# Kernel tuning notes

Measured on AMD Instinct MI355X. Metric: run time of the kernel, lower is better.

## Reference

```python
import jax, jax.numpy as jnp
import numpy as np

P, B, N, K = 8, 256, 512, 64
RHO = 0.999

def setup_inputs() -> dict:
    key = jax.random.key(0)
    k1, k2, k3, k4, k5, k6 = jax.random.split(key, 6)
    return {
        "WL": jax.random.normal(k1, (P, B, N, K), dtype=jnp.float32) * 0.05,
        "WR": jax.random.normal(k2, (P, B, K, N), dtype=jnp.float32) * 0.05,
        "v_tm1": jax.random.normal(k3, (B, N), dtype=jnp.float32),
        "v_t": jax.random.normal(k4, (B, N), dtype=jnp.float32),
        "ac_idx": jax.random.randint(k5, (B,), 0, P, dtype=jnp.int32),
        "pc_mask": jax.random.randint(k6, (B, P), 0, 2, dtype=jnp.int32),
    }

def reference(WL, WR, v_tm1, v_t, ac_idx, pc_mask):
    # constants from rehebbian(): n = x.shape[-1]*rho**2, g = 0.5*(log(1+r)-log(1-r))/r
    n = N * RHO ** 2
    g = 0.5 * (np.log(1.0 + RHO) - np.log(1.0 - RHO)) / RHO

    # ---- per-example pathway gather + batched low-rank matvec + tanh (tick v update) ----
    b_idx = jnp.arange(B)
    WL_sel = WL[ac_idx, b_idx]            # [B, N, K]
    WR_sel = WR[ac_idx, b_idx]            # [B, K, N]
    Wx = jnp.einsum("bkn,bn->bk", WR_sel, v_t)      # [B, K]
    v_next = jnp.tanh(jnp.einsum("bnk,bk->bn", WL_sel, Wx))  # [B, N]

    # ---- rehebbian rank-1 growth for every pathway, gated per example ----
    WRx = jnp.einsum("pbkn,bn->pbk", WR, v_tm1)      # [P, B, K]
    WLWRx = jnp.einsum("pbnk,pbk->pbn", WL, WRx)     # [P, B, N]
    mask = pc_mask.T.astype(WL.dtype)[:, :, None]    # [P, B, 1]
    dWL = ((g * v_t[None, :, :] - WLWRx) * mask)[..., None]          # [P, B, N, 1]
    dWR = (v_tm1[None, :, None, :] / n) * mask[..., None]            # [P, B, 1, N]
    return v_next, dWL, dWR
```

## Files before the change

kernel.cpp:

```cpp
#include <hip/hip_runtime.h>
#include <math.h>

#define GP 8
#define GB 256
#define GN 512
#define GK 64

__device__ __forceinline__ void fma4(float4& acc, const float4 a, const float4 b) {
    acc.x += a.x * b.x; acc.y += a.y * b.y; acc.z += a.z * b.z; acc.w += a.w * b.w;
}
__device__ __forceinline__ float hsum4(const float4 a) {
    return (a.x + a.y) + (a.z + a.w);
}

__global__ __launch_bounds__(256, 4) void ghu_fused(
    const float* __restrict__ WL,
    const float* __restrict__ WR,
    const float* __restrict__ v_tm1,
    const float* __restrict__ v_t,
    const int*   __restrict__ ac_idx,
    const int*   __restrict__ pc_mask,
    float* __restrict__ out,
    float g, float inv_n)
{
    const int b    = blockIdx.x;
    const int p    = blockIdx.y;
    const int tid  = threadIdx.x;
    const int wave = tid >> 6;
    const int lane = tid & 63;
    const int sub  = lane & 3;
    const int rsub = lane >> 2;

    __shared__ float s_vtm1[GN];
    __shared__ float s_vt[GN];
    __shared__ float s_WRx[GK];
    __shared__ float s_Wx[GK];
    __shared__ float s_dWL[GN];
    __shared__ float s_vnext[GN];

    s_vtm1[tid]       = v_tm1[b * GN + tid];
    s_vtm1[tid + 256] = v_tm1[b * GN + tid + 256];
    s_vt[tid]         = v_t[b * GN + tid];
    s_vt[tid + 256]   = v_t[b * GN + tid + 256];
    __syncthreads();

    const bool  sel   = (ac_idx[b] == p);
    const float maskv = (float)pc_mask[b * GP + p];

    const float4* sv_u  = (const float4*)s_vtm1;
    const float4* sv_t4 = (const float4*)s_vt;

    {
        const float4* WR4  = (const float4*)(WR + (size_t)(p * GB + b) * (GK * GN));
        const int     k    = wave * 16 + rsub;
        const float4* rowp = WR4 + k * 128 + sub;

        float4 accA[2], accB[2];
        accA[0] = accA[1] = make_float4(0.f, 0.f, 0.f, 0.f);
        accB[0] = accB[1] = make_float4(0.f, 0.f, 0.f, 0.f);
        #pragma unroll
        for (int j = 0; j < 32; ++j) {
            const float4 a = rowp[4 * j];
            const float4 u = sv_u[sub + 4 * j];
            const float4 t = sv_t4[sub + 4 * j];
            fma4(accA[j & 1], a, u);
            fma4(accB[j & 1], a, t);
        }
        float wrx = hsum4(accA[0]) + hsum4(accA[1]);
        float wx  = hsum4(accB[0]) + hsum4(accB[1]);
        wrx += __shfl_xor(wrx, 1);
        wrx += __shfl_xor(wrx, 2);
        wx  += __shfl_xor(wx, 1);
        wx  += __shfl_xor(wx, 2);
        if (sub == 0) {
            s_WRx[k] = wrx;
            s_Wx[k]  = wx;
        }
    }
    __syncthreads();

    {
        float4 wr4[4], wx4[4];
        #pragma unroll
        for (int j = 0; j < 4; ++j) {
            wr4[j] = ((const float4*)s_WRx)[sub + 4 * j];
            wx4[j] = ((const float4*)s_Wx)[sub + 4 * j];
        }

        const float4* WL4 = (const float4*)(WL + (size_t)(p * GB + b) * (GN * GK));
        #pragma unroll
        for (int i = 0; i < 8; ++i) {
            const int     n  = i * 64 + wave * 16 + rsub;
            const float4* rp = WL4 + n * 16 + sub;
            const float4 a0 = rp[0];
            const float4 a1 = rp[4];
            const float4 a2 = rp[8];
            const float4 a3 = rp[12];

            float4 dacc = make_float4(0.f, 0.f, 0.f, 0.f);
            fma4(dacc, a0, wr4[0]); fma4(dacc, a1, wr4[1]);
            fma4(dacc, a2, wr4[2]); fma4(dacc, a3, wr4[3]);
            float d = hsum4(dacc);
            d += __shfl_xor(d, 1);
            d += __shfl_xor(d, 2);

            if (sel) {
                float4 dacc2 = make_float4(0.f, 0.f, 0.f, 0.f);
                fma4(dacc2, a0, wx4[0]); fma4(dacc2, a1, wx4[1]);
                fma4(dacc2, a2, wx4[2]); fma4(dacc2, a3, wx4[3]);
                float d2 = hsum4(dacc2);
                d2 += __shfl_xor(d2, 1);
                d2 += __shfl_xor(d2, 2);
                if (sub == 0) s_vnext[n] = tanhf(d2);
            }
            if (sub == 0) s_dWL[n] = (g * s_vt[n] - d) * maskv;
        }
    }
    __syncthreads();

    const size_t pbN = (size_t)(p * GB + b) * GN;
    float* dWL_out = out + (size_t)GB * GN + pbN;
    float* dWR_out = out + (size_t)GB * GN + (size_t)GP * GB * GN + pbN;

    dWL_out[tid]       = s_dWL[tid];
    dWL_out[tid + 256] = s_dWL[tid + 256];

    const float sc = maskv * inv_n;
    dWR_out[tid]       = s_vtm1[tid] * sc;
    dWR_out[tid + 256] = s_vtm1[tid + 256] * sc;

    if (sel) {
        out[b * GN + tid]       = s_vnext[tid];
        out[b * GN + tid + 256] = s_vnext[tid + 256];
    }
}

extern "C" void kernel_launch(void* const* d_in, const int* in_sizes, int n_in,
                              void* d_out, int out_size, void* d_ws, size_t ws_size,
                              hipStream_t stream) {
    const float* WL     = (const float*)d_in[0];
    const float* WR     = (const float*)d_in[1];
    const float* v_tm1  = (const float*)d_in[2];
    const float* v_t    = (const float*)d_in[3];
    const int*   ac_idx = (const int*)d_in[4];
    const int*   pc_msk = (const int*)d_in[5];
    float* out = (float*)d_out;

    const double RHO = 0.999;
    const float g     = (float)(0.5 * (log(1.0 + RHO) - log(1.0 - RHO)) / RHO);
    const float inv_n = (float)(1.0 / ((double)GN * RHO * RHO));

    dim3 grid(GB, GP);
    ghu_fused<<<grid, 256, 0, stream>>>(WL, WR, v_tm1, v_t, ac_idx, pc_msk,
                                        out, g, inv_n);
}
```

Baseline: 514.1 us.

## Remap matvec threads so each wave reads full contiguous rows, skip unused Wx work

Rewrites the thread mapping for both low-rank matvecs so a whole wave reads contiguous float4 rows of WR and WL, with the activation vector held in registers instead of shared memory. Row sums now use 64-lane or 16-lane shuffle reductions instead of 4-lane ones. The v_t products are computed only for the selected pathway, and the shared staging of v_tm1 and its first barrier are removed. In exchange there are many more shuffle operations per row, and the loops load fewer rows at a time, so fewer memory requests may be in flight.

```diff
diff --git a/kernel.cpp b/kernel.cpp
--- a/kernel.cpp
+++ b/kernel.cpp
@@ -11,6 +11,16 @@
 }
 __device__ __forceinline__ float hsum4(const float4 a) {
     return (a.x + a.y) + (a.z + a.w);
+}
+__device__ __forceinline__ float reduce64(float s) {
+    s += __shfl_xor(s, 1);  s += __shfl_xor(s, 2);  s += __shfl_xor(s, 4);
+    s += __shfl_xor(s, 8);  s += __shfl_xor(s, 16); s += __shfl_xor(s, 32);
+    return s;
+}
+__device__ __forceinline__ float reduce16(float s) {
+    s += __shfl_xor(s, 1); s += __shfl_xor(s, 2);
+    s += __shfl_xor(s, 4); s += __shfl_xor(s, 8);
+    return s;
 }
 
 __global__ __launch_bounds__(256, 4) void ghu_fused(
@@ -28,92 +38,87 @@
     const int tid  = threadIdx.x;
     const int wave = tid >> 6;
     const int lane = tid & 63;
-    const int sub  = lane & 3;
-    const int rsub = lane >> 2;
 
-    __shared__ float s_vtm1[GN];
     __shared__ float s_vt[GN];
     __shared__ float s_WRx[GK];
     __shared__ float s_Wx[GK];
     __shared__ float s_dWL[GN];
     __shared__ float s_vnext[GN];
 
-    s_vtm1[tid]       = v_tm1[b * GN + tid];
-    s_vtm1[tid + 256] = v_tm1[b * GN + tid + 256];
-    s_vt[tid]         = v_t[b * GN + tid];
-    s_vt[tid + 256]   = v_t[b * GN + tid + 256];
-    __syncthreads();
-
     const bool  sel   = (ac_idx[b] == p);
     const float maskv = (float)pc_mask[b * GP + p];
 
-    const float4* sv_u  = (const float4*)s_vtm1;
-    const float4* sv_t4 = (const float4*)s_vt;
+    const float4* v4u = (const float4*)(v_tm1 + b * GN);
+    const float4* v4t = (const float4*)(v_t   + b * GN);
+
+    if (tid < 128) ((float4*)s_vt)[tid] = v4t[tid];
 
     {
-        const float4* WR4  = (const float4*)(WR + (size_t)(p * GB + b) * (GK * GN));
-        const int     k    = wave * 16 + rsub;
-        const float4* rowp = WR4 + k * 128 + sub;
+        const float4 vu_lo = v4u[lane];
+        const float4 vu_hi = v4u[64 + lane];
+        float4 vt_lo, vt_hi;
+        if (sel) { vt_lo = v4t[lane]; vt_hi = v4t[64 + lane]; }
 
-        float4 accA[2], accB[2];
-        accA[0] = accA[1] = make_float4(0.f, 0.f, 0.f, 0.f);
-        accB[0] = accB[1] = make_float4(0.f, 0.f, 0.f, 0.f);
-        #pragma unroll
-        for (int j = 0; j < 32; ++j) {
-            const float4 a = rowp[4 * j];
-            const float4 u = sv_u[sub + 4 * j];
-            const float4 t = sv_t4[sub + 4 * j];
-            fma4(accA[j & 1], a, u);
-            fma4(accB[j & 1], a, t);
-        }
-        float wrx = hsum4(accA[0]) + hsum4(accA[1]);
-        float wx  = hsum4(accB[0]) + hsum4(accB[1]);
-        wrx += __shfl_xor(wrx, 1);
-        wrx += __shfl_xor(wrx, 2);
-        wx  += __shfl_xor(wx, 1);
-        wx  += __shfl_xor(wx, 2);
-        if (sub == 0) {
-            s_WRx[k] = wrx;
-            s_Wx[k]  = wx;
+        const float4* WR4 = (const float4*)(WR + (size_t)(p * GB + b) * (GK * GN));
+        const int k0 = wave * 16;
+
+        for (int rr = 0; rr < 16; rr += 4) {
+            float4 a[8];
+            #pragma unroll
+            for (int j = 0; j < 4; ++j) {
+                const int k = k0 + rr + j;
+                a[2 * j]     = WR4[k * 128 + lane];
+                a[2 * j + 1] = WR4[k * 128 + 64 + lane];
+            }
+            #pragma unroll
+            for (int j = 0; j < 4; ++j) {
+                const int k = k0 + rr + j;
+                float4 acc = make_float4(0.f, 0.f, 0.f, 0.f);
+                fma4(acc, a[2 * j],     vu_lo);
+                fma4(acc, a[2 * j + 1], vu_hi);
+                const float s = reduce64(hsum4(acc));
+                if (lane == 0) s_WRx[k] = s;
+                if (sel) {
+                    float4 acc2 = make_float4(0.f, 0.f, 0.f, 0.f);
+                    fma4(acc2, a[2 * j],     vt_lo);
+                    fma4(acc2, a[2 * j + 1], vt_hi);
+                    const float s2 = reduce64(hsum4(acc2));
+                    if (lane == 0) s_Wx[k] = s2;
+                }
+            }
         }
     }
     __syncthreads();
 
     {
-        float4 wr4[4], wx4[4];
-        #pragma unroll
-        for (int j = 0; j < 4; ++j) {
-            wr4[j] = ((const float4*)s_WRx)[sub + 4 * j];
-            wx4[j] = ((const float4*)s_Wx)[sub + 4 * j];
-        }
+        const float4 wrx = ((const float4*)s_WRx)[lane & 15];
+        float4 wx;
+        if (sel) wx = ((const float4*)s_Wx)[lane & 15];
 
         const float4* WL4 = (const float4*)(WL + (size_t)(p * GB + b) * (GN * GK));
-        #pragma unroll
-        for (int i = 0; i < 8; ++i) {
-            const int     n  = i * 64 + wave * 16 + rsub;
-            const float4* rp = WL4 + n * 16 + sub;
-            const float4 a0 = rp[0];
-            const float4 a1 = rp[4];
-            const float4 a2 = rp[8];
-            const float4 a3 = rp[12];
+        const int sub = lane >> 4;
 
-            float4 dacc = make_float4(0.f, 0.f, 0.f, 0.f);
-            fma4(dacc, a0, wr4[0]); fma4(dacc, a1, wr4[1]);
-            fma4(dacc, a2, wr4[2]); fma4(dacc, a3, wr4[3]);
-            float d = hsum4(dacc);
-            d += __shfl_xor(d, 1);
-            d += __shfl_xor(d, 2);
-
-            if (sel) {
-                float4 dacc2 = make_float4(0.f, 0.f, 0.f, 0.f);
-                fma4(dacc2, a0, wx4[0]); fma4(dacc2, a1, wx4[1]);
-                fma4(dacc2, a2, wx4[2]); fma4(dacc2, a3, wx4[3]);
-                float d2 = hsum4(dacc2);
-                d2 += __shfl_xor(d2, 1);
-                d2 += __shfl_xor(d2, 2);
-                if (sub == 0) s_vnext[n] = tanhf(d2);
+        for (int it = 0; it < 4; ++it) {
+            const int n0 = wave * 128 + it * 32;
+            float4 a[8];
+            #pragma unroll
+            for (int j = 0; j < 8; ++j) {
+                a[j] = WL4[(n0 + 4 * j) * 16 + lane];
             }
-            if (sub == 0) s_dWL[n] = (g * s_vt[n] - d) * maskv;
+            #pragma unroll
+            for (int j = 0; j < 8; ++j) {
+                const int n = n0 + 4 * j + sub;
+                float4 acc = make_float4(0.f, 0.f, 0.f, 0.f);
+                fma4(acc, a[j], wrx);
+                const float d = reduce16(hsum4(acc));
+                if ((lane & 15) == 0) s_dWL[n] = (g * s_vt[n] - d) * maskv;
+                if (sel) {
+                    float4 acc2 = make_float4(0.f, 0.f, 0.f, 0.f);
+                    fma4(acc2, a[j], wx);
+                    const float d2 = reduce16(hsum4(acc2));
+                    if ((lane & 15) == 0) s_vnext[n] = tanhf(d2);
+                }
+            }
         }
     }
     __syncthreads();
@@ -126,8 +131,8 @@
     dWL_out[tid + 256] = s_dWL[tid + 256];
 
     const float sc = maskv * inv_n;
-    dWR_out[tid]       = s_vtm1[tid] * sc;
-    dWR_out[tid + 256] = s_vtm1[tid + 256] * sc;
+    dWR_out[tid]       = v_tm1[b * GN + tid] * sc;
+    dWR_out[tid + 256] = v_tm1[b * GN + tid + 256] * sc;
 
     if (sel) {
         out[b * GN + tid]       = s_vnext[tid];
```

After: 516.4 us. About the same (+0.5%).
